# Performance work log

Measured on AMD Instinct MI355X. Metric: run time of the kernel, lower is better.

Reference implementation:

```python
import jax, jax.numpy as jnp
import numpy as np

B, F, D = 16384, 256, 128
H = [512, 256]
OUT = 8
VOCAB = 100000


def setup_inputs() -> dict:
    key = jax.random.key(0)
    ks = jax.random.split(key, 16)
    s = lambda k, *sh: jax.random.normal(k, sh, jnp.float32) * 0.05
    return dict(
        features=jax.random.normal(ks[0], (B, F), jnp.float32),
        ent_idx=jax.random.randint(ks[1], (B,), 0, VOCAB),
        target=jax.random.randint(ks[2], (B,), 0, OUT),
        Wf=s(ks[3], F, D), bf=jnp.zeros((D,), jnp.float32),
        Wu=s(ks[4], D, D), bu=jnp.zeros((D,), jnp.float32),
        w_cf=s(ks[5], D), w_fc=s(ks[6], D),
        w_ef=s(ks[7], D), w_fe=s(ks[8], D),
        b_c=jnp.zeros((1,), jnp.float32), b_e=jnp.zeros((1,), jnp.float32),
        head_tab=s(ks[9], VOCAB, D), ent_tab=s(ks[10], VOCAB, D),
        W0=s(ks[11], 2 * D, H[0]), b0=jnp.zeros((H[0],), jnp.float32),
        W1=s(ks[12], H[0], H[1]), b1=jnp.zeros((H[1],), jnp.float32),
        W2=s(ks[13], H[1], OUT), b2=jnp.zeros((OUT,), jnp.float32),
    )


def cross_compress(f, e, w_cf, w_fc, w_ef, w_fe, b_c, b_e):
    # torch code builds c = f (outer) e of shape (B,D,D) then matmuls a (D,1)
    # vector; algebraically (f e^T) w = f * (e . w), so we use the O(B*D) form.
    ew_cf = e @ w_cf  # (B,)
    fw_fc = f @ w_fc
    ew_ef = e @ w_ef
    fw_fe = f @ w_fe
    new_f = f * ew_cf[:, None] + e * fw_fc[:, None] + b_c
    new_e = f * ew_ef[:, None] + e * fw_fe[:, None] + b_e
    return new_f, new_e


def reference(features, ent_idx, target, Wf, bf, Wu, bu, w_cf, w_fc, w_ef,
              w_fe, b_c, b_e, head_tab, ent_tab, W0, b0, W1, b1, W2, b2):
    # 'rec' branch of CompanyOperationEvaluation.forward (eval mode, dropout=id)
    cf = jax.nn.relu(features @ Wf + bf)          # feature_layer
    e = ent_tab[ent_idx]                           # entity_embed lookup
    h = head_tab[ent_idx]                          # head_embed lookup (same ids)
    for _ in range(2):
        cf = jax.nn.relu(cf @ Wu + bu)             # user_low_mlp_layer
        h, e = cross_compress(h, e, w_cf, w_fc, w_ef, w_fe, b_c, b_e)
    high = jnp.concatenate([cf, e], axis=1)        # (B, 2D)
    x = jax.nn.relu(high @ W0 + b0)
    x = jax.nn.relu(x @ W1 + b1)
    x = jax.nn.relu(x @ W2 + b2)                   # pred_last_layer
    prob = jax.nn.softmax(x, axis=1)
    return (prob, target)
```

## Files before the change

### kernel.cpp

```cpp
#include <hip/hip_runtime.h>
#include <hip/hip_bf16.h>


typedef __bf16 bf16x8 __attribute__((ext_vector_type(8)));
typedef float floatx4 __attribute__((ext_vector_type(4)));

__device__ __forceinline__ unsigned short f2bf(float x) {
  unsigned int u = __builtin_bit_cast(unsigned int, x);
  u = (u + 0x7FFFu + ((u >> 16) & 1u)) >> 16;
  return (unsigned short)u;
}

#define PHASE_BAR()                                      \
  do {                                                   \
    asm volatile("s_waitcnt lgkmcnt(0)" ::: "memory");   \
    __builtin_amdgcn_s_barrier();                        \
    __builtin_amdgcn_sched_barrier(0);                   \
  } while (0)

__global__ __launch_bounds__(256) void prep_kernel(
    const float* __restrict__ Wf, const float* __restrict__ Wu,
    const float* __restrict__ W0, const float* __restrict__ W1,
    const float* __restrict__ W2,
    unsigned short* __restrict__ wfT, unsigned short* __restrict__ wuT,
    unsigned short* __restrict__ w0T, unsigned short* __restrict__ w1T,
    unsigned short* __restrict__ w2T) {
  __shared__ unsigned short tile[32][34];
  const int bid = blockIdx.x, tid = threadIdx.x;
  if (bid < 304) {
    int t = bid;
    const float* src; unsigned short* dst; int N, K, kt, nt;
    if (t < 32)       { src = Wf; dst = wfT; N = 128; K = 256; kt = t >> 2;       nt = t & 3; }
    else if (t < 48)  { t -= 32;  src = Wu; dst = wuT; N = 128; K = 128; kt = t >> 2; nt = t & 3; }
    else if (t < 176) { t -= 48;  src = W0; dst = w0T; N = 512; K = 256; kt = t >> 4; nt = t & 15; }
    else              { t -= 176; src = W1; dst = w1T; N = 256; K = 512; kt = t >> 3; nt = t & 7; }
    {
      int r = tid >> 3, cg = (tid & 7) * 4;
      float4 v = *(const float4*)(src + (size_t)(kt * 32 + r) * N + nt * 32 + cg);
      tile[r][cg + 0] = f2bf(v.x); tile[r][cg + 1] = f2bf(v.y);
      tile[r][cg + 2] = f2bf(v.z); tile[r][cg + 3] = f2bf(v.w);
    }
    __syncthreads();
    {
      int rp = tid >> 3, cg = (tid & 7) * 4;
      uint2 o;
      o.x = (unsigned)tile[cg + 0][rp] | ((unsigned)tile[cg + 1][rp] << 16);
      o.y = (unsigned)tile[cg + 2][rp] | ((unsigned)tile[cg + 3][rp] << 16);
      *(uint2*)(dst + (size_t)(nt * 32 + rp) * K + kt * 32 + cg) = o;
    }
  } else {
#pragma unroll
    for (int i = 0; i < 8; ++i) {
      int g = tid * 8 + i, k = g >> 3, n = g & 7;
      w2T[n * 256 + k] = f2bf(W2[g]);
    }
  }
}

template <int LDK>
__device__ __forceinline__ void loadB(uint4 (&r)[4],
                                      const unsigned short* __restrict__ p,
                                      int tid) {
#pragma unroll
  for (int i = 0; i < 4; ++i) {
    int chunk = i * 256 + tid, row = chunk >> 3, seg = chunk & 7;
    r[i] = *(const uint4*)(p + (size_t)row * LDK + seg * 8);
  }
}

__device__ __forceinline__ void dsw(unsigned short* b, const uint4 (&r)[4],
                                    int tid) {
#pragma unroll
  for (int i = 0; i < 4; ++i) {
    int chunk = i * 256 + tid, row = chunk >> 3, seg = chunk & 7;
    *(uint4*)&b[row * 72 + seg * 8] = r[i];
  }
}

template <int PASS_STEPS, int LDK>
__device__ __forceinline__ const unsigned short* srcstep(
    const unsigned short* __restrict__ s, int st) {
  return s + (size_t)(st / PASS_STEPS) * 128 * LDK + (st % PASS_STEPS) * 64;
}

template <int LDA>
__device__ __forceinline__ void mstep(const unsigned short* A,
                                      const unsigned short* b, int k0,
                                      floatx4* acc, int m16, int quad,
                                      int wave) {
#pragma unroll
  for (int kk = 0; kk < 64; kk += 32) {
    bf16x8 a0 = *(const bf16x8*)&A[m16 * LDA + k0 + kk + quad * 8];
    bf16x8 a1 = *(const bf16x8*)&A[(16 + m16) * LDA + k0 + kk + quad * 8];
    bf16x8 b0 = *(const bf16x8*)&b[(wave * 32 + m16) * 72 + kk + quad * 8];
    bf16x8 b1 = *(const bf16x8*)&b[(wave * 32 + 16 + m16) * 72 + kk + quad * 8];
    acc[0] = __builtin_amdgcn_mfma_f32_16x16x32_bf16(a0, b0, acc[0], 0, 0, 0);
    acc[1] = __builtin_amdgcn_mfma_f32_16x16x32_bf16(a0, b1, acc[1], 0, 0, 0);
    acc[2] = __builtin_amdgcn_mfma_f32_16x16x32_bf16(a1, b0, acc[2], 0, 0, 0);
    acc[3] = __builtin_amdgcn_mfma_f32_16x16x32_bf16(a1, b1, acc[3], 0, 0, 0);
  }
}

template <int T, int LDA, int PASS_STEPS, int LDK>
__device__ __forceinline__ void gemm_phase(
    const unsigned short* A, const unsigned short* __restrict__ src,
    unsigned short* b_sh, floatx4* acc, int tid, int m16, int quad, int wave) {
  uint4 r[3][4];
  loadB<LDK>(r[0], srcstep<PASS_STEPS, LDK>(src, 0), tid);
  dsw(b_sh, r[0], tid);
  if (T > 1) loadB<LDK>(r[1], srcstep<PASS_STEPS, LDK>(src, 1), tid);
  if (T > 2) loadB<LDK>(r[2], srcstep<PASS_STEPS, LDK>(src, 2), tid);
  PHASE_BAR();
#pragma unroll
  for (int t = 0; t < T; ++t) {
    if (t + 3 < T)
      loadB<LDK>(r[t % 3], srcstep<PASS_STEPS, LDK>(src, t + 3), tid);
    mstep<LDA>(A, b_sh + (t & 1) * 9216, (t % PASS_STEPS) * 64,
               acc + (t / PASS_STEPS) * 4, m16, quad, wave);
    if (t + 1 < T) dsw(b_sh + ((t + 1) & 1) * 9216, r[(t + 1) % 3], tid);
    PHASE_BAR();
  }
}

__global__ __launch_bounds__(256, 2) void fused_mlp_kernel(
    const float* __restrict__ features, const int* __restrict__ ent_idx,
    const float* __restrict__ head_tab, const float* __restrict__ ent_tab,
    const float* __restrict__ w_cf, const float* __restrict__ w_fc,
    const float* __restrict__ w_ef, const float* __restrict__ w_fe,
    const float* __restrict__ b_c, const float* __restrict__ b_e,
    const unsigned short* __restrict__ wfT,
    const unsigned short* __restrict__ wuT, const float* __restrict__ bf_,
    const float* __restrict__ bu,
    const unsigned short* __restrict__ w0T, const float* __restrict__ b0,
    const unsigned short* __restrict__ w1T, const float* __restrict__ b1,
    const unsigned short* __restrict__ w2T, const float* __restrict__ b2,
    const int* __restrict__ target, float* __restrict__ out) {
  __shared__ __align__(16) unsigned short regionA[17152];
  __shared__ __align__(16) unsigned short b_sh[2 * 9216];
  __shared__ __align__(16) unsigned short w2_sh[2048];
  __shared__ __align__(16) float cw_sh[512];
  unsigned short* feat_sh = regionA;
  unsigned short* buf0 = regionA + 8448;
  unsigned short* buf1 = regionA + 12800;
  unsigned short* A_sh = regionA;
  unsigned short* x0_sh = regionA;
  unsigned short* x1_sh = b_sh;

  const int tid = threadIdx.x;
  const int r0 = blockIdx.x * 32;
  const int lane = tid & 63, wave = tid >> 6;
  const int m16 = lane & 15, quad = lane >> 4;

  const int grow = tid >> 3, gpart = tid & 7;
  const int gidx = ent_idx[r0 + grow];
  const float* hp = head_tab + (size_t)gidx * 128 + gpart * 16;
  const float* ep = ent_tab + (size_t)gidx * 128 + gpart * 16;
  float4 h4[4], e4[4];
#pragma unroll
  for (int j = 0; j < 4; ++j) {
    h4[j] = *(const float4*)(hp + j * 4);
    e4[j] = *(const float4*)(ep + j * 4);
  }
  if (tid < 128) {
    int a = tid >> 5, o = (tid & 31) * 4;
    const float* s = (a == 0) ? w_cf : (a == 1) ? w_fc : (a == 2) ? w_ef : w_fe;
    *(float4*)&cw_sh[a * 128 + o] = *(const float4*)(s + o);
  }
  *(uint4*)&w2_sh[tid * 8] = *(const uint4*)(w2T + tid * 8);

#pragma unroll
  for (int i = 0; i < 8; ++i) {
    int idx4 = i * 256 + tid;
    int row = idx4 >> 6, c = (idx4 & 63) * 4;
    float4 v = *(const float4*)(features + (size_t)(r0 + row) * 256 + c);
    uint2 o;
    o.x = (unsigned)f2bf(v.x) | ((unsigned)f2bf(v.y) << 16);
    o.y = (unsigned)f2bf(v.z) | ((unsigned)f2bf(v.w) << 16);
    *(uint2*)&feat_sh[row * 264 + c] = o;
  }

  floatx4 acc[4];
#pragma unroll
  for (int j = 0; j < 4; ++j) acc[j] = (floatx4){0.f, 0.f, 0.f, 0.f};
  gemm_phase<4, 264, 4, 256>(feat_sh, wfT, b_sh, acc, tid, m16, quad, wave);
#pragma unroll
  for (int mi = 0; mi < 2; ++mi)
#pragma unroll
    for (int ni = 0; ni < 2; ++ni) {
      int col = wave * 32 + ni * 16 + m16;
      float bv = bf_[col];
#pragma unroll
      for (int r = 0; r < 4; ++r)
        buf0[(mi * 16 + quad * 4 + r) * 136 + col] =
            f2bf(fmaxf(acc[mi * 2 + ni][r] + bv, 0.f));
    }

  {
    float h[16], e[16];
#pragma unroll
    for (int j = 0; j < 4; ++j) {
      h[4 * j + 0] = h4[j].x; h[4 * j + 1] = h4[j].y;
      h[4 * j + 2] = h4[j].z; h[4 * j + 3] = h4[j].w;
      e[4 * j + 0] = e4[j].x; e[4 * j + 1] = e4[j].y;
      e[4 * j + 2] = e4[j].z; e[4 * j + 3] = e4[j].w;
    }
    const float bc = b_c[0], be = b_e[0];
#pragma unroll
    for (int it = 0; it < 2; ++it) {
      float d0 = 0.f, d1 = 0.f, d2 = 0.f, d3 = 0.f;
#pragma unroll
      for (int j = 0; j < 16; ++j) {
        float wcf = cw_sh[0 * 128 + gpart * 16 + j];
        float wfc = cw_sh[1 * 128 + gpart * 16 + j];
        float wef = cw_sh[2 * 128 + gpart * 16 + j];
        float wfe = cw_sh[3 * 128 + gpart * 16 + j];
        d0 += e[j] * wcf; d1 += h[j] * wfc;
        d2 += e[j] * wef; d3 += h[j] * wfe;
      }
#pragma unroll
      for (int s = 1; s < 8; s <<= 1) {
        d0 += __shfl_xor(d0, s); d1 += __shfl_xor(d1, s);
        d2 += __shfl_xor(d2, s); d3 += __shfl_xor(d3, s);
      }
#pragma unroll
      for (int j = 0; j < 16; ++j) {
        float nh = h[j] * d0 + e[j] * d1 + bc;
        float ne = h[j] * d2 + e[j] * d3 + be;
        h[j] = nh; e[j] = ne;
      }
    }
    uint4 o0, o1;
    unsigned* w = (unsigned*)&o0;
#pragma unroll
    for (int j = 0; j < 4; ++j)
      w[j] = (unsigned)f2bf(e[2 * j]) | ((unsigned)f2bf(e[2 * j + 1]) << 16);
    w = (unsigned*)&o1;
#pragma unroll
    for (int j = 0; j < 4; ++j)
      w[j] = (unsigned)f2bf(e[8 + 2 * j]) |
             ((unsigned)f2bf(e[8 + 2 * j + 1]) << 16);
    *(uint4*)&A_sh[grow * 264 + 128 + gpart * 16] = o0;
    *(uint4*)&A_sh[grow * 264 + 128 + gpart * 16 + 8] = o1;
  }

#pragma unroll
  for (int j = 0; j < 4; ++j) acc[j] = (floatx4){0.f, 0.f, 0.f, 0.f};
  gemm_phase<2, 136, 2, 128>(buf0, wuT, b_sh, acc, tid, m16, quad, wave);
#pragma unroll
  for (int mi = 0; mi < 2; ++mi)
#pragma unroll
    for (int ni = 0; ni < 2; ++ni) {
      int col = wave * 32 + ni * 16 + m16;
      float bv = bu[col];
#pragma unroll
      for (int r = 0; r < 4; ++r)
        buf1[(mi * 16 + quad * 4 + r) * 136 + col] =
            f2bf(fmaxf(acc[mi * 2 + ni][r] + bv, 0.f));
    }

#pragma unroll
  for (int j = 0; j < 4; ++j) acc[j] = (floatx4){0.f, 0.f, 0.f, 0.f};
  PHASE_BAR();
  mstep<136>(buf1, b_sh, 0, acc, m16, quad, wave);
  mstep<136>(buf1, b_sh + 9216, 64, acc, m16, quad, wave);
  PHASE_BAR();
#pragma unroll
  for (int mi = 0; mi < 2; ++mi)
#pragma unroll
    for (int ni = 0; ni < 2; ++ni) {
      int col = wave * 32 + ni * 16 + m16;
      float bv = bu[col];
#pragma unroll
      for (int r = 0; r < 4; ++r)
        A_sh[(mi * 16 + quad * 4 + r) * 264 + col] =
            f2bf(fmaxf(acc[mi * 2 + ni][r] + bv, 0.f));
    }

  floatx4 acc16[16];
#pragma unroll
  for (int j = 0; j < 16; ++j) acc16[j] = (floatx4){0.f, 0.f, 0.f, 0.f};
  gemm_phase<16, 264, 4, 256>(A_sh, w0T, b_sh, acc16, tid, m16, quad, wave);
#pragma unroll
  for (int np = 0; np < 4; ++np)
#pragma unroll
    for (int mi = 0; mi < 2; ++mi)
#pragma unroll
      for (int ni = 0; ni < 2; ++ni) {
        int col = np * 128 + wave * 32 + ni * 16 + m16;
        float bv = b0[col];
#pragma unroll
        for (int r = 0; r < 4; ++r)
          x0_sh[(mi * 16 + quad * 4 + r) * 520 + col] =
              f2bf(fmaxf(acc16[np * 4 + mi * 2 + ni][r] + bv, 0.f));
      }

  floatx4 acc8[8];
#pragma unroll
  for (int j = 0; j < 8; ++j) acc8[j] = (floatx4){0.f, 0.f, 0.f, 0.f};
  gemm_phase<16, 520, 8, 512>(x0_sh, w1T, b_sh, acc8, tid, m16, quad, wave);
#pragma unroll
  for (int np = 0; np < 2; ++np)
#pragma unroll
    for (int mi = 0; mi < 2; ++mi)
#pragma unroll
      for (int ni = 0; ni < 2; ++ni) {
        int col = np * 128 + wave * 32 + ni * 16 + m16;
        float bv = b1[col];
#pragma unroll
        for (int r = 0; r < 4; ++r)
          x1_sh[(mi * 16 + quad * 4 + r) * 264 + col] =
              f2bf(fmaxf(acc8[np * 4 + mi * 2 + ni][r] + bv, 0.f));
      }
  PHASE_BAR();

  {
    int row = tid >> 3, q = tid & 7;
    float p[8];
#pragma unroll
    for (int n = 0; n < 8; ++n) p[n] = 0.f;
#pragma unroll
    for (int jb = 0; jb < 4; ++jb) {
      bf16x8 xv = *(const bf16x8*)&x1_sh[row * 264 + q * 32 + jb * 8];
#pragma unroll
      for (int n = 0; n < 8; ++n) {
        bf16x8 wv = *(const bf16x8*)&w2_sh[n * 256 + q * 32 + jb * 8];
#pragma unroll
        for (int j = 0; j < 8; ++j) p[n] += (float)xv[j] * (float)wv[j];
      }
    }
#pragma unroll
    for (int s = 1; s < 8; s <<= 1)
#pragma unroll
      for (int n = 0; n < 8; ++n) p[n] += __shfl_xor(p[n], s);
    if (q == 0) {
      float mx = -1e30f;
#pragma unroll
      for (int n = 0; n < 8; ++n) {
        p[n] = fmaxf(p[n] + b2[n], 0.f);
        mx = fmaxf(mx, p[n]);
      }
      float sum = 0.f;
#pragma unroll
      for (int n = 0; n < 8; ++n) { p[n] = __expf(p[n] - mx); sum += p[n]; }
      const float inv = 1.f / sum;
      const int gr = r0 + row;
      float4 o0 = {p[0] * inv, p[1] * inv, p[2] * inv, p[3] * inv};
      float4 o1 = {p[4] * inv, p[5] * inv, p[6] * inv, p[7] * inv};
      *(float4*)(out + (size_t)gr * 8) = o0;
      *(float4*)(out + (size_t)gr * 8 + 4) = o1;
      out[16384 * 8 + gr] = (float)target[gr];
    }
  }
}

extern "C" void kernel_launch(void* const* d_in, const int* in_sizes, int n_in,
                              void* d_out, int out_size, void* d_ws, size_t ws_size,
                              hipStream_t stream) {
  const float* features = (const float*)d_in[0];
  const int* ent_idx    = (const int*)d_in[1];
  const int* target     = (const int*)d_in[2];
  const float* Wf  = (const float*)d_in[3];
  const float* bf_ = (const float*)d_in[4];
  const float* Wu  = (const float*)d_in[5];
  const float* bu  = (const float*)d_in[6];
  const float* w_cf = (const float*)d_in[7];
  const float* w_fc = (const float*)d_in[8];
  const float* w_ef = (const float*)d_in[9];
  const float* w_fe = (const float*)d_in[10];
  const float* b_c  = (const float*)d_in[11];
  const float* b_e  = (const float*)d_in[12];
  const float* head_tab = (const float*)d_in[13];
  const float* ent_tab  = (const float*)d_in[14];
  const float* W0 = (const float*)d_in[15];
  const float* b0 = (const float*)d_in[16];
  const float* W1 = (const float*)d_in[17];
  const float* b1 = (const float*)d_in[18];
  const float* W2 = (const float*)d_in[19];
  const float* b2 = (const float*)d_in[20];
  float* out = (float*)d_out;

  unsigned short* ws = (unsigned short*)d_ws;
  size_t off = 0;
  auto alloc = [&](size_t n) { unsigned short* p = ws + off; off += n; return p; };
  unsigned short* wfT  = alloc(32768);
  unsigned short* wuT  = alloc(16384);
  unsigned short* w0T  = alloc(131072);
  unsigned short* w1T  = alloc(131072);
  unsigned short* w2T  = alloc(2048);
  (void)ws_size; (void)in_sizes; (void)n_in; (void)out_size;

  prep_kernel<<<305, 256, 0, stream>>>(Wf, Wu, W0, W1, W2,
                                       wfT, wuT, w0T, w1T, w2T);
  fused_mlp_kernel<<<512, 256, 0, stream>>>(features, ent_idx, head_tab,
      ent_tab, w_cf, w_fc, w_ef, w_fe, b_c, b_e, wfT, wuT, bf_, bu,
      w0T, b0, w1T, b1, w2T, b2, target, out);
}
```

Baseline: 184.9 us.

## Double rows per block to 64 with 2x4 wave grid sharing weight tiles

Each block now has 512 threads and processes 64 rows instead of 32, with the 8 waves arranged as 2 row groups by 4 column groups. Every weight tile staged in shared memory is therefore reused by twice as many rows, which roughly halves global and L2 weight traffic per row and the staging work per thread. In exchange, per-block LDS use roughly doubles and the grid shrinks to 256 blocks, one per CU. That leaves fewer independent blocks to hide load latency and barrier stalls.

```diff
diff --git a/kernel.cpp b/kernel.cpp
--- a/kernel.cpp
+++ b/kernel.cpp
@@ -58,21 +58,21 @@
 }
 
 template <int LDK>
-__device__ __forceinline__ void loadB(uint4 (&r)[4],
+__device__ __forceinline__ void loadB(uint4 (&r)[2],
                                       const unsigned short* __restrict__ p,
                                       int tid) {
 #pragma unroll
-  for (int i = 0; i < 4; ++i) {
-    int chunk = i * 256 + tid, row = chunk >> 3, seg = chunk & 7;
+  for (int i = 0; i < 2; ++i) {
+    int chunk = i * 512 + tid, row = chunk >> 3, seg = chunk & 7;
     r[i] = *(const uint4*)(p + (size_t)row * LDK + seg * 8);
   }
 }
 
-__device__ __forceinline__ void dsw(unsigned short* b, const uint4 (&r)[4],
+__device__ __forceinline__ void dsw(unsigned short* b, const uint4 (&r)[2],
                                     int tid) {
 #pragma unroll
-  for (int i = 0; i < 4; ++i) {
-    int chunk = i * 256 + tid, row = chunk >> 3, seg = chunk & 7;
+  for (int i = 0; i < 2; ++i) {
+    int chunk = i * 512 + tid, row = chunk >> 3, seg = chunk & 7;
     *(uint4*)&b[row * 72 + seg * 8] = r[i];
   }
 }
@@ -87,13 +87,13 @@
 __device__ __forceinline__ void mstep(const unsigned short* A,
                                       const unsigned short* b, int k0,
                                       floatx4* acc, int m16, int quad,
-                                      int wave) {
+                                      int wm, int wn) {
 #pragma unroll
   for (int kk = 0; kk < 64; kk += 32) {
-    bf16x8 a0 = *(const bf16x8*)&A[m16 * LDA + k0 + kk + quad * 8];
-    bf16x8 a1 = *(const bf16x8*)&A[(16 + m16) * LDA + k0 + kk + quad * 8];
-    bf16x8 b0 = *(const bf16x8*)&b[(wave * 32 + m16) * 72 + kk + quad * 8];
-    bf16x8 b1 = *(const bf16x8*)&b[(wave * 32 + 16 + m16) * 72 + kk + quad * 8];
+    bf16x8 a0 = *(const bf16x8*)&A[(wm * 32 + m16) * LDA + k0 + kk + quad * 8];
+    bf16x8 a1 = *(const bf16x8*)&A[(wm * 32 + 16 + m16) * LDA + k0 + kk + quad * 8];
+    bf16x8 b0 = *(const bf16x8*)&b[(wn * 32 + m16) * 72 + kk + quad * 8];
+    bf16x8 b1 = *(const bf16x8*)&b[(wn * 32 + 16 + m16) * 72 + kk + quad * 8];
     acc[0] = __builtin_amdgcn_mfma_f32_16x16x32_bf16(a0, b0, acc[0], 0, 0, 0);
     acc[1] = __builtin_amdgcn_mfma_f32_16x16x32_bf16(a0, b1, acc[1], 0, 0, 0);
     acc[2] = __builtin_amdgcn_mfma_f32_16x16x32_bf16(a1, b0, acc[2], 0, 0, 0);
@@ -104,8 +104,9 @@
 template <int T, int LDA, int PASS_STEPS, int LDK>
 __device__ __forceinline__ void gemm_phase(
     const unsigned short* A, const unsigned short* __restrict__ src,
-    unsigned short* b_sh, floatx4* acc, int tid, int m16, int quad, int wave) {
-  uint4 r[3][4];
+    unsigned short* b_sh, floatx4* acc, int tid, int m16, int quad, int wm,
+    int wn) {
+  uint4 r[3][2];
   loadB<LDK>(r[0], srcstep<PASS_STEPS, LDK>(src, 0), tid);
   dsw(b_sh, r[0], tid);
   if (T > 1) loadB<LDK>(r[1], srcstep<PASS_STEPS, LDK>(src, 1), tid);
@@ -116,13 +117,13 @@
     if (t + 3 < T)
       loadB<LDK>(r[t % 3], srcstep<PASS_STEPS, LDK>(src, t + 3), tid);
     mstep<LDA>(A, b_sh + (t & 1) * 9216, (t % PASS_STEPS) * 64,
-               acc + (t / PASS_STEPS) * 4, m16, quad, wave);
+               acc + (t / PASS_STEPS) * 4, m16, quad, wm, wn);
     if (t + 1 < T) dsw(b_sh + ((t + 1) & 1) * 9216, r[(t + 1) % 3], tid);
     PHASE_BAR();
   }
 }
 
-__global__ __launch_bounds__(256, 2) void fused_mlp_kernel(
+__global__ __launch_bounds__(512, 2) void fused_mlp_kernel(
     const float* __restrict__ features, const int* __restrict__ ent_idx,
     const float* __restrict__ head_tab, const float* __restrict__ ent_tab,
     const float* __restrict__ w_cf, const float* __restrict__ w_fc,
@@ -135,21 +136,22 @@
     const unsigned short* __restrict__ w1T, const float* __restrict__ b1,
     const unsigned short* __restrict__ w2T, const float* __restrict__ b2,
     const int* __restrict__ target, float* __restrict__ out) {
-  __shared__ __align__(16) unsigned short regionA[17152];
+  __shared__ __align__(16) unsigned short regionA[34304];
   __shared__ __align__(16) unsigned short b_sh[2 * 9216];
   __shared__ __align__(16) unsigned short w2_sh[2048];
   __shared__ __align__(16) float cw_sh[512];
   unsigned short* feat_sh = regionA;
-  unsigned short* buf0 = regionA + 8448;
-  unsigned short* buf1 = regionA + 12800;
+  unsigned short* buf0 = regionA + 16896;
+  unsigned short* buf1 = regionA + 25600;
   unsigned short* A_sh = regionA;
   unsigned short* x0_sh = regionA;
   unsigned short* x1_sh = b_sh;
 
   const int tid = threadIdx.x;
-  const int r0 = blockIdx.x * 32;
+  const int r0 = blockIdx.x * 64;
   const int lane = tid & 63, wave = tid >> 6;
   const int m16 = lane & 15, quad = lane >> 4;
+  const int wm = wave >> 2, wn = wave & 3;
 
   const int grow = tid >> 3, gpart = tid & 7;
   const int gidx = ent_idx[r0 + grow];
@@ -166,11 +168,11 @@
     const float* s = (a == 0) ? w_cf : (a == 1) ? w_fc : (a == 2) ? w_ef : w_fe;
     *(float4*)&cw_sh[a * 128 + o] = *(const float4*)(s + o);
   }
-  *(uint4*)&w2_sh[tid * 8] = *(const uint4*)(w2T + tid * 8);
+  if (tid < 256) *(uint4*)&w2_sh[tid * 8] = *(const uint4*)(w2T + tid * 8);
 
 #pragma unroll
   for (int i = 0; i < 8; ++i) {
-    int idx4 = i * 256 + tid;
+    int idx4 = i * 512 + tid;
     int row = idx4 >> 6, c = (idx4 & 63) * 4;
     float4 v = *(const float4*)(features + (size_t)(r0 + row) * 256 + c);
     uint2 o;
@@ -182,16 +184,16 @@
   floatx4 acc[4];
 #pragma unroll
   for (int j = 0; j < 4; ++j) acc[j] = (floatx4){0.f, 0.f, 0.f, 0.f};
-  gemm_phase<4, 264, 4, 256>(feat_sh, wfT, b_sh, acc, tid, m16, quad, wave);
+  gemm_phase<4, 264, 4, 256>(feat_sh, wfT, b_sh, acc, tid, m16, quad, wm, wn);
 #pragma unroll
   for (int mi = 0; mi < 2; ++mi)
 #pragma unroll
     for (int ni = 0; ni < 2; ++ni) {
-      int col = wave * 32 + ni * 16 + m16;
+      int col = wn * 32 + ni * 16 + m16;
       float bv = bf_[col];
 #pragma unroll
       for (int r = 0; r < 4; ++r)
-        buf0[(mi * 16 + quad * 4 + r) * 136 + col] =
+        buf0[(wm * 32 + mi * 16 + quad * 4 + r) * 136 + col] =
             f2bf(fmaxf(acc[mi * 2 + ni][r] + bv, 0.f));
     }
 
@@ -245,70 +247,70 @@
 
 #pragma unroll
   for (int j = 0; j < 4; ++j) acc[j] = (floatx4){0.f, 0.f, 0.f, 0.f};
-  gemm_phase<2, 136, 2, 128>(buf0, wuT, b_sh, acc, tid, m16, quad, wave);
+  gemm_phase<2, 136, 2, 128>(buf0, wuT, b_sh, acc, tid, m16, quad, wm, wn);
 #pragma unroll
   for (int mi = 0; mi < 2; ++mi)
 #pragma unroll
     for (int ni = 0; ni < 2; ++ni) {
-      int col = wave * 32 + ni * 16 + m16;
+      int col = wn * 32 + ni * 16 + m16;
       float bv = bu[col];
 #pragma unroll
       for (int r = 0; r < 4; ++r)
-        buf1[(mi * 16 + quad * 4 + r) * 136 + col] =
+        buf1[(wm * 32 + mi * 16 + quad * 4 + r) * 136 + col] =
             f2bf(fmaxf(acc[mi * 2 + ni][r] + bv, 0.f));
     }
 
 #pragma unroll
   for (int j = 0; j < 4; ++j) acc[j] = (floatx4){0.f, 0.f, 0.f, 0.f};
   PHASE_BAR();
-  mstep<136>(buf1, b_sh, 0, acc, m16, quad, wave);
-  mstep<136>(buf1, b_sh + 9216, 64, acc, m16, quad, wave);
+  mstep<136>(buf1, b_sh, 0, acc, m16, quad, wm, wn);
+  mstep<136>(buf1, b_sh + 9216, 64, acc, m16, quad, wm, wn);
   PHASE_BAR();
 #pragma unroll
   for (int mi = 0; mi < 2; ++mi)
 #pragma unroll
     for (int ni = 0; ni < 2; ++ni) {
-      int col = wave * 32 + ni * 16 + m16;
+      int col = wn * 32 + ni * 16 + m16;
       float bv = bu[col];
 #pragma unroll
       for (int r = 0; r < 4; ++r)
-        A_sh[(mi * 16 + quad * 4 + r) * 264 + col] =
+        A_sh[(wm * 32 + mi * 16 + quad * 4 + r) * 264 + col] =
             f2bf(fmaxf(acc[mi * 2 + ni][r] + bv, 0.f));
     }
 
   floatx4 acc16[16];
 #pragma unroll
   for (int j = 0; j < 16; ++j) acc16[j] = (floatx4){0.f, 0.f, 0.f, 0.f};
-  gemm_phase<16, 264, 4, 256>(A_sh, w0T, b_sh, acc16, tid, m16, quad, wave);
+  gemm_phase<16, 264, 4, 256>(A_sh, w0T, b_sh, acc16, tid, m16, quad, wm, wn);
 #pragma unroll
   for (int np = 0; np < 4; ++np)
 #pragma unroll
     for (int mi = 0; mi < 2; ++mi)
 #pragma unroll
       for (int ni = 0; ni < 2; ++ni) {
-        int col = np * 128 + wave * 32 + ni * 16 + m16;
+        int col = np * 128 + wn * 32 + ni * 16 + m16;
         float bv = b0[col];
 #pragma unroll
         for (int r = 0; r < 4; ++r)
-          x0_sh[(mi * 16 + quad * 4 + r) * 520 + col] =
+          x0_sh[(wm * 32 + mi * 16 + quad * 4 + r) * 520 + col] =
               f2bf(fmaxf(acc16[np * 4 + mi * 2 + ni][r] + bv, 0.f));
       }
 
   floatx4 acc8[8];
 #pragma unroll
   for (int j = 0; j < 8; ++j) acc8[j] = (floatx4){0.f, 0.f, 0.f, 0.f};
-  gemm_phase<16, 520, 8, 512>(x0_sh, w1T, b_sh, acc8, tid, m16, quad, wave);
+  gemm_phase<16, 520, 8, 512>(x0_sh, w1T, b_sh, acc8, tid, m16, quad, wm, wn);
 #pragma unroll
   for (int np = 0; np < 2; ++np)
 #pragma unroll
     for (int mi = 0; mi < 2; ++mi)
 #pragma unroll
       for (int ni = 0; ni < 2; ++ni) {
-        int col = np * 128 + wave * 32 + ni * 16 + m16;
+        int col = np * 128 + wn * 32 + ni * 16 + m16;
         float bv = b1[col];
 #pragma unroll
         for (int r = 0; r < 4; ++r)
-          x1_sh[(mi * 16 + quad * 4 + r) * 264 + col] =
+          x1_sh[(wm * 32 + mi * 16 + quad * 4 + r) * 264 + col] =
               f2bf(fmaxf(acc8[np * 4 + mi * 2 + ni][r] + bv, 0.f));
       }
   PHASE_BAR();
@@ -391,7 +393,7 @@
 
   prep_kernel<<<305, 256, 0, stream>>>(Wf, Wu, W0, W1, W2,
                                        wfT, wuT, w0T, w1T, w2T);
-  fused_mlp_kernel<<<512, 256, 0, stream>>>(features, ent_idx, head_tab,
+  fused_mlp_kernel<<<256, 512, 0, stream>>>(features, ent_idx, head_tab,
       ent_tab, w_cf, w_fc, w_ef, w_fe, b_c, b_e, wfT, wuT, bf_, bu,
       w0T, b0, w1T, b1, w2T, b2, target, out);
 }
```

Result: slower. 190.8 us (+3.2%).

## Stage weight tiles via global_load_lds with XOR-swizzled unpadded LDS layout

Applied to the files above, without the earlier changes.

Replaces register-staged B tile loads (global load into VGPRs, then ds_write) with direct global-to-LDS loads via __builtin_amdgcn_global_load_lds. Padded LDS strides are replaced by an XOR swizzle on all A and B buffers, which shrinks LDS use. Prefetch depth drops from three tiles in registers to one tile ahead in a double buffer, and the barrier now also waits on vmcnt. The aim is to cut VGPR pressure and LDS write instructions, at the risk of exposing global load latency with the shallower prefetch. Note that x1_sh still uses stride 264 within b_sh, and b_sh has shrunk, so those writes may not fit or may alias.

```diff
diff --git a/kernel.cpp b/kernel.cpp
--- a/kernel.cpp
+++ b/kernel.cpp
@@ -11,11 +11,15 @@
   return (unsigned short)u;
 }
 
-#define PHASE_BAR()                                      \
-  do {                                                   \
-    asm volatile("s_waitcnt lgkmcnt(0)" ::: "memory");   \
-    __builtin_amdgcn_s_barrier();                        \
-    __builtin_amdgcn_sched_barrier(0);                   \
+__device__ __forceinline__ int sz(int row, int col) {
+  return col ^ ((row & 7) << 3);
+}
+
+#define PHASE_BAR()                                                  \
+  do {                                                               \
+    asm volatile("s_waitcnt vmcnt(0) lgkmcnt(0)" ::: "memory");      \
+    __builtin_amdgcn_s_barrier();                                    \
+    __builtin_amdgcn_sched_barrier(0);                               \
   } while (0)
 
 __global__ __launch_bounds__(256) void prep_kernel(
@@ -58,22 +62,18 @@
 }
 
 template <int LDK>
-__device__ __forceinline__ void loadB(uint4 (&r)[4],
-                                      const unsigned short* __restrict__ p,
-                                      int tid) {
+__device__ __forceinline__ void stageB(unsigned short* dstbase,
+                                       const unsigned short* __restrict__ src,
+                                       int tid) {
 #pragma unroll
   for (int i = 0; i < 4; ++i) {
-    int chunk = i * 256 + tid, row = chunk >> 3, seg = chunk & 7;
-    r[i] = *(const uint4*)(p + (size_t)row * LDK + seg * 8);
-  }
-}
-
-__device__ __forceinline__ void dsw(unsigned short* b, const uint4 (&r)[4],
-                                    int tid) {
-#pragma unroll
-  for (int i = 0; i < 4; ++i) {
-    int chunk = i * 256 + tid, row = chunk >> 3, seg = chunk & 7;
-    *(uint4*)&b[row * 72 + seg * 8] = r[i];
+    int chunk = i * 256 + tid;
+    int row = chunk >> 3, segs = chunk & 7;
+    int segl = segs ^ (row & 7);
+    const unsigned short* g = src + (size_t)row * LDK + segl * 8;
+    unsigned short* d = dstbase + chunk * 8;
+    __builtin_amdgcn_global_load_lds((const unsigned int*)g, (unsigned int*)d,
+                                     16, 0, 0);
   }
 }
 
@@ -85,15 +85,19 @@
 
 template <int LDA>
 __device__ __forceinline__ void mstep(const unsigned short* A,
-                                      const unsigned short* b, int k0,
+                                      const unsigned short* bt, int k0,
                                       floatx4* acc, int m16, int quad,
                                       int wave) {
 #pragma unroll
   for (int kk = 0; kk < 64; kk += 32) {
-    bf16x8 a0 = *(const bf16x8*)&A[m16 * LDA + k0 + kk + quad * 8];
-    bf16x8 a1 = *(const bf16x8*)&A[(16 + m16) * LDA + k0 + kk + quad * 8];
-    bf16x8 b0 = *(const bf16x8*)&b[(wave * 32 + m16) * 72 + kk + quad * 8];
-    bf16x8 b1 = *(const bf16x8*)&b[(wave * 32 + 16 + m16) * 72 + kk + quad * 8];
+    const int ca = k0 + kk + quad * 8;
+    const int cb = kk + quad * 8;
+    const int ra0 = m16, ra1 = 16 + m16;
+    const int rb0 = wave * 32 + m16, rb1 = wave * 32 + 16 + m16;
+    bf16x8 a0 = *(const bf16x8*)&A[ra0 * LDA + sz(ra0, ca)];
+    bf16x8 a1 = *(const bf16x8*)&A[ra1 * LDA + sz(ra1, ca)];
+    bf16x8 b0 = *(const bf16x8*)&bt[rb0 * 64 + sz(rb0, cb)];
+    bf16x8 b1 = *(const bf16x8*)&bt[rb1 * 64 + sz(rb1, cb)];
     acc[0] = __builtin_amdgcn_mfma_f32_16x16x32_bf16(a0, b0, acc[0], 0, 0, 0);
     acc[1] = __builtin_amdgcn_mfma_f32_16x16x32_bf16(a0, b1, acc[1], 0, 0, 0);
     acc[2] = __builtin_amdgcn_mfma_f32_16x16x32_bf16(a1, b0, acc[2], 0, 0, 0);
@@ -105,19 +109,15 @@
 __device__ __forceinline__ void gemm_phase(
     const unsigned short* A, const unsigned short* __restrict__ src,
     unsigned short* b_sh, floatx4* acc, int tid, int m16, int quad, int wave) {
-  uint4 r[3][4];
-  loadB<LDK>(r[0], srcstep<PASS_STEPS, LDK>(src, 0), tid);
-  dsw(b_sh, r[0], tid);
-  if (T > 1) loadB<LDK>(r[1], srcstep<PASS_STEPS, LDK>(src, 1), tid);
-  if (T > 2) loadB<LDK>(r[2], srcstep<PASS_STEPS, LDK>(src, 2), tid);
+  stageB<LDK>(b_sh, srcstep<PASS_STEPS, LDK>(src, 0), tid);
   PHASE_BAR();
 #pragma unroll
   for (int t = 0; t < T; ++t) {
-    if (t + 3 < T)
-      loadB<LDK>(r[t % 3], srcstep<PASS_STEPS, LDK>(src, t + 3), tid);
-    mstep<LDA>(A, b_sh + (t & 1) * 9216, (t % PASS_STEPS) * 64,
+    if (t + 1 < T)
+      stageB<LDK>(b_sh + ((t + 1) & 1) * 8192,
+                  srcstep<PASS_STEPS, LDK>(src, t + 1), tid);
+    mstep<LDA>(A, b_sh + (t & 1) * 8192, (t % PASS_STEPS) * 64,
                acc + (t / PASS_STEPS) * 4, m16, quad, wave);
-    if (t + 1 < T) dsw(b_sh + ((t + 1) & 1) * 9216, r[(t + 1) % 3], tid);
     PHASE_BAR();
   }
 }
@@ -135,13 +135,13 @@
     const unsigned short* __restrict__ w1T, const float* __restrict__ b1,
     const unsigned short* __restrict__ w2T, const float* __restrict__ b2,
     const int* __restrict__ target, float* __restrict__ out) {
-  __shared__ __align__(16) unsigned short regionA[17152];
-  __shared__ __align__(16) unsigned short b_sh[2 * 9216];
+  __shared__ __align__(16) unsigned short regionA[16384];
+  __shared__ __align__(16) unsigned short b_sh[2 * 8192];
   __shared__ __align__(16) unsigned short w2_sh[2048];
   __shared__ __align__(16) float cw_sh[512];
   unsigned short* feat_sh = regionA;
-  unsigned short* buf0 = regionA + 8448;
-  unsigned short* buf1 = regionA + 12800;
+  unsigned short* buf0 = regionA + 8192;
+  unsigned short* buf1 = regionA + 12288;
   unsigned short* A_sh = regionA;
   unsigned short* x0_sh = regionA;
   unsigned short* x1_sh = b_sh;
@@ -176,13 +176,13 @@
     uint2 o;
     o.x = (unsigned)f2bf(v.x) | ((unsigned)f2bf(v.y) << 16);
     o.y = (unsigned)f2bf(v.z) | ((unsigned)f2bf(v.w) << 16);
-    *(uint2*)&feat_sh[row * 264 + c] = o;
+    *(uint2*)&feat_sh[row * 256 + sz(row, c)] = o;
   }
 
   floatx4 acc[4];
 #pragma unroll
   for (int j = 0; j < 4; ++j) acc[j] = (floatx4){0.f, 0.f, 0.f, 0.f};
-  gemm_phase<4, 264, 4, 256>(feat_sh, wfT, b_sh, acc, tid, m16, quad, wave);
+  gemm_phase<4, 256, 4, 256>(feat_sh, wfT, b_sh, acc, tid, m16, quad, wave);
 #pragma unroll
   for (int mi = 0; mi < 2; ++mi)
 #pragma unroll
@@ -190,9 +190,11 @@
       int col = wave * 32 + ni * 16 + m16;
       float bv = bf_[col];
 #pragma unroll
-      for (int r = 0; r < 4; ++r)
-        buf0[(mi * 16 + quad * 4 + r) * 136 + col] =
+      for (int r = 0; r < 4; ++r) {
+        int row = mi * 16 + quad * 4 + r;
+        buf0[row * 128 + sz(row, col)] =
             f2bf(fmaxf(acc[mi * 2 + ni][r] + bv, 0.f));
+      }
     }
 
   {
@@ -239,13 +241,14 @@
     for (int j = 0; j < 4; ++j)
       w[j] = (unsigned)f2bf(e[8 + 2 * j]) |
              ((unsigned)f2bf(e[8 + 2 * j + 1]) << 16);
-    *(uint4*)&A_sh[grow * 264 + 128 + gpart * 16] = o0;
-    *(uint4*)&A_sh[grow * 264 + 128 + gpart * 16 + 8] = o1;
+    const int c0 = 128 + gpart * 16;
+    *(uint4*)&A_sh[grow * 256 + sz(grow, c0)] = o0;
+    *(uint4*)&A_sh[grow * 256 + sz(grow, c0 + 8)] = o1;
   }
 
 #pragma unroll
   for (int j = 0; j < 4; ++j) acc[j] = (floatx4){0.f, 0.f, 0.f, 0.f};
-  gemm_phase<2, 136, 2, 128>(buf0, wuT, b_sh, acc, tid, m16, quad, wave);
+  gemm_phase<2, 128, 2, 128>(buf0, wuT, b_sh, acc, tid, m16, quad, wave);
 #pragma unroll
   for (int mi = 0; mi < 2; ++mi)
 #pragma unroll
@@ -253,16 +256,18 @@
       int col = wave * 32 + ni * 16 + m16;
       float bv = bu[col];
 #pragma unroll
-      for (int r = 0; r < 4; ++r)
-        buf1[(mi * 16 + quad * 4 + r) * 136 + col] =
+      for (int r = 0; r < 4; ++r) {
+        int row = mi * 16 + quad * 4 + r;
+        buf1[row * 128 + sz(row, col)] =
             f2bf(fmaxf(acc[mi * 2 + ni][r] + bv, 0.f));
+      }
     }
 
 #pragma unroll
   for (int j = 0; j < 4; ++j) acc[j] = (floatx4){0.f, 0.f, 0.f, 0.f};
   PHASE_BAR();
-  mstep<136>(buf1, b_sh, 0, acc, m16, quad, wave);
-  mstep<136>(buf1, b_sh + 9216, 64, acc, m16, quad, wave);
+  mstep<128>(buf1, b_sh, 0, acc, m16, quad, wave);
+  mstep<128>(buf1, b_sh + 8192, 64, acc, m16, quad, wave);
   PHASE_BAR();
 #pragma unroll
   for (int mi = 0; mi < 2; ++mi)
@@ -271,15 +276,17 @@
       int col = wave * 32 + ni * 16 + m16;
       float bv = bu[col];
 #pragma unroll
-      for (int r = 0; r < 4; ++r)
-        A_sh[(mi * 16 + quad * 4 + r) * 264 + col] =
+      for (int r = 0; r < 4; ++r) {
+        int row = mi * 16 + quad * 4 + r;
+        A_sh[row * 256 + sz(row, col)] =
             f2bf(fmaxf(acc[mi * 2 + ni][r] + bv, 0.f));
+      }
     }
 
   floatx4 acc16[16];
 #pragma unroll
   for (int j = 0; j < 16; ++j) acc16[j] = (floatx4){0.f, 0.f, 0.f, 0.f};
-  gemm_phase<16, 264, 4, 256>(A_sh, w0T, b_sh, acc16, tid, m16, quad, wave);
+  gemm_phase<16, 256, 4, 256>(A_sh, w0T, b_sh, acc16, tid, m16, quad, wave);
 #pragma unroll
   for (int np = 0; np < 4; ++np)
 #pragma unroll
@@ -289,15 +296,17 @@
         int col = np * 128 + wave * 32 + ni * 16 + m16;
         float bv = b0[col];
 #pragma unroll
-        for (int r = 0; r < 4; ++r)
-          x0_sh[(mi * 16 + quad * 4 + r) * 520 + col] =
+        for (int r = 0; r < 4; ++r) {
+          int row = mi * 16 + quad * 4 + r;
+          x0_sh[row * 512 + sz(row, col)] =
               f2bf(fmaxf(acc16[np * 4 + mi * 2 + ni][r] + bv, 0.f));
+        }
       }
 
   floatx4 acc8[8];
 #pragma unroll
   for (int j = 0; j < 8; ++j) acc8[j] = (floatx4){0.f, 0.f, 0.f, 0.f};
-  gemm_phase<16, 520, 8, 512>(x0_sh, w1T, b_sh, acc8, tid, m16, quad, wave);
+  gemm_phase<16, 512, 8, 512>(x0_sh, w1T, b_sh, acc8, tid, m16, quad, wave);
 #pragma unroll
   for (int np = 0; np < 2; ++np)
 #pragma unroll
```

Measured after the change: 185.2 us. Within noise of the previous version (+0.2%).
